# Performance work log

Hardware: AMD Instinct MI355X
Metric: run time of the kernel (lower is better)

The kernel has to match this reference:

```python
import jax, jax.numpy as jnp
import numpy as np

B, LV, HW, LT, D, H = 4, 16, 196, 32, 768, 12
DH = D // H
SCALE = 1.0 / np.sqrt(DH).astype(np.float32)


def _lin(x, W, b):
    # torch nn.Linear convention: W is [out, in]
    return x @ W.T + b


def _split_heads(x):
    # (..., D) -> (..., H, DH)
    return x.reshape(*x.shape[:-1], H, DH)


def _attn_logits(feat_q, feat_k, mask_q, mask_k, Wq, bq, Wk, bk):
    # feat_q: (B, LV, Lq, D), feat_k: (B, LV, Lk, D)
    q = _split_heads(_lin(feat_q, Wq, bq))  # b v q h d
    k = _split_heads(_lin(feat_k, Wk, bk))  # b v k h d
    logits = jnp.einsum('bvqhd,bvkhd->bvhqk', q, k)
    m = (mask_q[:, :, None] & mask_k[:, None, :])[:, None, None]  # b 1 1 q k
    return jnp.where(m, logits, -10000.0)


def setup_inputs() -> dict:
    key = jax.random.key(0)
    ks = jax.random.split(key, 12)
    inp = {
        'vid_feat': jax.random.normal(ks[0], (B, LV, HW, D), jnp.float32),
        'txt_feat': jax.random.normal(ks[1], (B, LV, LT, D), jnp.float32),
        'vid_mask': jnp.ones((B, LV), dtype=bool),
        'txt_mask': jax.random.randint(ks[2], (B, LT), 0, 2) > 0,
    }
    for i, name in enumerate(['v2v', 't2v', 't2t', 'v2t']):
        inp[name + '_W'] = jax.random.normal(ks[3 + 2 * i], (3, D, D), jnp.float32) * 0.02
        inp[name + '_b'] = jnp.zeros((3, D), jnp.float32)
    return inp


def reference(vid_feat, txt_feat, vid_mask, txt_mask,
              v2v_W, v2v_b, t2v_W, t2v_b, t2t_W, t2t_b, v2t_W, v2t_b):
    mask_hw = jnp.ones((vid_feat.shape[0], HW), dtype=bool)

    # values: concat video-keys then text-keys along the key axis
    v_value = jnp.concatenate([_lin(vid_feat, v2v_W[2], v2v_b[2]),
                               _lin(txt_feat, t2v_W[2], t2v_b[2])], axis=2)
    v_value = _split_heads(v_value)  # b v (HW+LT) h d
    t_value = jnp.concatenate([_lin(vid_feat, v2t_W[2], v2t_b[2]),
                               _lin(txt_feat, t2t_W[2], t2t_b[2])], axis=2)
    t_value = _split_heads(t_value)

    # logits (source call order: get_attn_logits(feat_k, mask_k, feat_q, mask_q, ...))
    v2v = _attn_logits(vid_feat, vid_feat, mask_hw, mask_hw, v2v_W[0], v2v_b[0], v2v_W[1], v2v_b[1])
    t2v = _attn_logits(vid_feat, txt_feat, mask_hw, txt_mask, t2v_W[0], t2v_b[0], t2v_W[1], t2v_b[1])
    v2t = _attn_logits(txt_feat, vid_feat, txt_mask, mask_hw, v2t_W[0], v2t_b[0], v2t_W[1], v2t_b[1])
    t2t = _attn_logits(txt_feat, txt_feat, txt_mask, txt_mask, t2t_W[0], t2t_b[0], t2t_W[1], t2t_b[1])

    v_logits = jnp.concatenate([v2v, t2v], axis=-1)  # b v h HW (HW+LT)
    t_logits = jnp.concatenate([v2t, t2t], axis=-1)  # b v h LT (HW+LT)

    # NOTE: source scales probabilities AFTER softmax by 1/sqrt(d_head)
    vid_out = jnp.einsum('bvhqk,bvkhd->bvqhd', jax.nn.softmax(v_logits, axis=-1) * SCALE, v_value)
    vid_out = vid_out.reshape(*vid_out.shape[:3], D)
    txt_out = jnp.einsum('bvhqk,bvkhd->bvqhd', jax.nn.softmax(t_logits, axis=-1) * SCALE, t_value)
    txt_out = txt_out.reshape(*txt_out.shape[:3], D)
    return (vid_out, txt_out)
```

## Files before the change

kernel.cpp:

```cpp
#include <hip/hip_runtime.h>

#define NBV 64
#define HWN 196
#define LTN 32
#define DIM 768
#define NH 12
#define DHD 64
#define ATT_SCALE 0.125f

typedef __attribute__((ext_vector_type(8))) __bf16 bf16x8;
typedef __attribute__((ext_vector_type(4))) float f32x4;

static __device__ __forceinline__ unsigned short f2bf(float f) {
    union { float f; unsigned u; } v; v.f = f;
    unsigned r = v.u + 0x7FFFu + ((v.u >> 16) & 1u);
    return (unsigned short)(r >> 16);
}

#define MFMA16(a, b, c) __builtin_amdgcn_mfma_f32_16x16x32_bf16((a), (b), (c), 0, 0, 0)
#define GLOAD_LDS16(g, l)                                                      \
    __builtin_amdgcn_global_load_lds(                                          \
        (const __attribute__((address_space(1))) void*)(g),                    \
        (__attribute__((address_space(3))) void*)(l), 16, 0, 0)

struct CvtCfg {
    const float* src[14];
    unsigned short* dst[14];
    int n4[14];
};

__global__ __launch_bounds__(256) void cvt_bf16(CvtCfg cfg) {
    const int e = blockIdx.y;
    const float4* s = (const float4*)cfg.src[e];
    unsigned short* d = cfg.dst[e];
    const int n4 = cfg.n4[e];
    for (int i = blockIdx.x * 256 + threadIdx.x; i < n4; i += gridDim.x * 256) {
        float4 v = s[i];
        ushort4 o;
        o.x = f2bf(v.x); o.y = f2bf(v.y); o.z = f2bf(v.z); o.w = f2bf(v.w);
        *(ushort4*)(d + (long)i * 4) = o;
    }
}

struct GemmCfg {
    const unsigned short* A[2];
    const unsigned short* W[2];
    unsigned short* out[2];
    const float* bias[2][6];
    int M[2];
};

__global__ __launch_bounds__(512, 2) void gemm_proj(GemmCfg cfg, int nb0)
{
    __shared__ __align__(16) unsigned short lds[65536];
    const int tid = threadIdx.x;
    const int lane = tid & 63, wid = tid >> 6;
    const int wm = wid >> 2, wn = wid & 3;
    const int fr = lane & 15, fg = lane >> 4;

    const int nwg = gridDim.x;
    const int orig = blockIdx.x;
    const int q = nwg >> 3, r = nwg & 7;
    const int xcd = orig & 7, lid = orig >> 3;
    const int wg = (xcd < r ? xcd * (q + 1) : r * (q + 1) + (xcd - r) * q) + lid;

    const int set = wg >= nb0;
    const int local = wg - (set ? nb0 : 0);
    const int mt = local / 18, nt = local - mt * 18;
    const int m0 = mt * 256, n0 = nt * 256;
    const int M = cfg.M[set];
    const unsigned short* __restrict__ A = cfg.A[set];
    const unsigned short* __restrict__ W = cfg.W[set];

    const int srow = tid >> 2;
    const int sxor = ((tid & 3) ^ ((tid >> 3) & 3)) * 8;
    const unsigned short* aSrc = A + (long)(m0 + srow) * DIM + sxor;
    const unsigned short* bSrc = W + (long)(n0 + srow) * DIM + sxor;
    unsigned short* ldst = lds + tid * 8;

    const int rxor = (fg ^ ((fr >> 1) & 3)) * 8;
    const int aoff = (wm * 128 + fr) * 32 + rxor;
    const int boff = 8192 + (wn * 64 + fr) * 32 + rxor;

    f32x4 acc[8][4] = {};

#define STAGE(t, s) do {                                                       \
    const unsigned short* _a = aSrc + (t) * 32;                                \
    const unsigned short* _b = bSrc + (t) * 32;                                \
    unsigned short* _d = ldst + (s) * 16384;                                   \
    GLOAD_LDS16(_a, _d);                                                       \
    GLOAD_LDS16(_a + 98304, _d + 4096);                                        \
    GLOAD_LDS16(_b, _d + 8192);                                                \
    GLOAD_LDS16(_b + 98304, _d + 12288);                                       \
} while (0)

#define COMPUTE(s) do {                                                        \
    const unsigned short* _sa = lds + (s) * 16384 + aoff;                      \
    const unsigned short* _sb = lds + (s) * 16384 + boff;                      \
    bf16x8 af[8], bg[4];                                                       \
    _Pragma("unroll") for (int m = 0; m < 4; ++m)                              \
        af[m] = *(const bf16x8*)(_sa + m * 512);                               \
    _Pragma("unroll") for (int n = 0; n < 4; ++n)                              \
        bg[n] = *(const bf16x8*)(_sb + n * 512);                               \
    _Pragma("unroll") for (int m = 4; m < 8; ++m)                              \
        af[m] = *(const bf16x8*)(_sa + m * 512);                               \
    __builtin_amdgcn_s_setprio(1);                                             \
    _Pragma("unroll") for (int m = 0; m < 4; ++m)                              \
    _Pragma("unroll") for (int n = 0; n < 4; ++n)                              \
        acc[m][n] = MFMA16(bg[n], af[m], acc[m][n]);                           \
    __builtin_amdgcn_s_setprio(0);                                             \
    __builtin_amdgcn_s_setprio(1);                                             \
    _Pragma("unroll") for (int m = 4; m < 8; ++m)                              \
    _Pragma("unroll") for (int n = 0; n < 4; ++n)                              \
        acc[m][n] = MFMA16(bg[n], af[m], acc[m][n]);                           \
    __builtin_amdgcn_s_setprio(0);                                             \
} while (0)

    STAGE(0, 0); STAGE(1, 1); STAGE(2, 2);
#pragma unroll 1
    for (int t = 0; t < 21; ++t) {
        asm volatile("s_waitcnt vmcnt(8)" ::: "memory");
        __builtin_amdgcn_s_barrier();
        STAGE(t + 3, (t + 3) & 3);
        COMPUTE(t & 3);
    }
    asm volatile("s_waitcnt vmcnt(8)" ::: "memory");
    __builtin_amdgcn_s_barrier();
    COMPUTE(1);
    asm volatile("s_waitcnt vmcnt(4)" ::: "memory");
    __builtin_amdgcn_s_barrier();
    COMPUTE(2);
    asm volatile("s_waitcnt vmcnt(0)" ::: "memory");
    __builtin_amdgcn_s_barrier();
    COMPUTE(3);

#undef STAGE
#undef COMPUTE

    const int w = nt / 3;
    const int nlb = (nt - w * 3) * 256;
    const float* bp = cfg.bias[set][w];
    unsigned short* op = cfg.out[set] + (long)w * M * DIM;
    const int colL = wn * 64;
    __builtin_amdgcn_s_barrier();
#pragma unroll
    for (int p = 0; p < 2; ++p) {
        if (wm == p) {
#pragma unroll
            for (int n = 0; n < 4; ++n) {
                float4 b4 = *(const float4*)(bp + nlb + colL + n * 16 + fg * 4);
#pragma unroll
                for (int m = 0; m < 8; ++m) {
                    ushort4 u;
                    u.x = f2bf(acc[m][n][0] + b4.x);
                    u.y = f2bf(acc[m][n][1] + b4.y);
                    u.z = f2bf(acc[m][n][2] + b4.z);
                    u.w = f2bf(acc[m][n][3] + b4.w);
                    *(ushort4*)&lds[(m * 16 + fr) * 264 + colL + n * 16 + fg * 4] = u;
                }
            }
        }
        __builtin_amdgcn_s_barrier();
#pragma unroll
        for (int i = 0; i < 8; ++i) {
            int chunk = tid + i * 512;
            int rr = chunk >> 5, cb = chunk & 31;
            bf16x8 v = *(const bf16x8*)&lds[rr * 264 + cb * 8];
            *(bf16x8*)(op + (long)(m0 + p * 128 + rr) * DIM + nlb + cb * 8) = v;
        }
        if (p == 0) __builtin_amdgcn_s_barrier();
    }
}

struct TransCfg {
    const unsigned short* src[4];
    unsigned short* dst[4];
};

__global__ __launch_bounds__(256) void transpose_v(TransCfg cfg)
{
    __shared__ unsigned short t[32][33];
    const int x = blockIdx.x;
    const int which = x >> 3;
    const int xi = x & 7;
    const int istxt = (xi == 7);
    const unsigned short* src = cfg.src[which * 2 + istxt];
    unsigned short* dst = cfg.dst[which];
    const int nrows = istxt ? LTN : HWN;
    const int colbase = istxt ? 208 : 0;
    const int rt = istxt ? 0 : xi;

    const int bv = blockIdx.z, dt = blockIdx.y;
    const int tx = threadIdx.x & 31, ty = threadIdx.x >> 5;
#pragma unroll
    for (int i = 0; i < 4; ++i) {
        int r = rt * 32 + ty + i * 8;
        t[ty + i * 8][tx] = (r < nrows)
            ? src[(long)(bv * nrows + r) * DIM + dt * 32 + tx] : (unsigned short)0;
    }
    __syncthreads();
#pragma unroll
    for (int i = 0; i < 4; ++i) {
        int d = dt * 32 + ty + i * 8;
        int rr = rt * 32 + tx;
        if (rr < nrows)
            dst[(long)(bv * DIM + d) * 256 + colbase + rr] = t[tx][ty + i * 8];
    }
}

struct AttnCfg {
    const unsigned short* QA[2];
    const unsigned short* QB[2];
    const unsigned short* KV[2];
    const unsigned short* KT[2];
    const unsigned short* Vt[2];
    float* outp[2];
};

__global__ __launch_bounds__(256, 2) void attn_kernel(AttnCfg cfg,
                                                      const int* __restrict__ tmask)
{
    __shared__ __align__(16) unsigned short P[4][16][256];
    const int tid = threadIdx.x, lane = tid & 63, wid = tid >> 6;
    const int bv = blockIdx.x, h = blockIdx.y;
    const int b = bv >> 4;
    const int sel = (blockIdx.z == 4);
    const int nq = sel ? LTN : HWN;
    const int qmask = sel;
    const unsigned short* QA = cfg.QA[sel];
    const unsigned short* QB = cfg.QB[sel];
    const unsigned short* KV = cfg.KV[sel];
    const unsigned short* KT = cfg.KT[sel];
    const unsigned short* Vt = cfg.Vt[sel];
    float* outp = cfg.outp[sel];
    const int q0 = (sel ? 0 : blockIdx.z * 64) + wid * 16;
    const int fr = lane & 15, fg = lane >> 4;

    int qr = q0 + fr; if (qr > nq - 1) qr = nq - 1;
    const unsigned short* qa_p = QA + (long)(bv * nq + qr) * DIM + h * DHD;
    const unsigned short* qb_p = QB + (long)(bv * nq + qr) * DIM + h * DHD;
    bf16x8 qa[2], qb[2];
#pragma unroll
    for (int kh = 0; kh < 2; ++kh) {
        qa[kh] = *(const bf16x8*)(qa_p + kh * 32 + fg * 8);
        qb[kh] = *(const bf16x8*)(qb_p + kh * 32 + fg * 8);
    }

    f32x4 acc[15];
#pragma unroll
    for (int kb = 0; kb < 13; ++kb) {
        int kr = kb * 16 + fr; if (kr > HWN - 1) kr = HWN - 1;
        const unsigned short* kp = KV + (long)(bv * HWN + kr) * DIM + h * DHD;
        f32x4 c = {0.f, 0.f, 0.f, 0.f};
        c = MFMA16(qa[0], *(const bf16x8*)(kp + fg * 8), c);
        c = MFMA16(qa[1], *(const bf16x8*)(kp + 32 + fg * 8), c);
        acc[kb] = c;
    }
#pragma unroll
    for (int kb = 13; kb < 15; ++kb) {
        int kr = (kb - 13) * 16 + fr;
        const unsigned short* kp = KT + (long)(bv * LTN + kr) * DIM + h * DHD;
        f32x4 c = {0.f, 0.f, 0.f, 0.f};
        c = MFMA16(qb[0], *(const bf16x8*)(kp + fg * 8), c);
        c = MFMA16(qb[1], *(const bf16x8*)(kp + 32 + fg * 8), c);
        acc[kb] = c;
    }

    bool vq[4];
#pragma unroll
    for (int j = 0; j < 4; ++j) {
        int qq = q0 + fg * 4 + j;
        if (qmask) { int qc = qq < LTN ? qq : LTN - 1; vq[j] = tmask[b * LTN + qc] != 0; }
        else vq[j] = true;
    }
#pragma unroll
    for (int kb = 0; kb < 15; ++kb) {
        int c = kb * 16 + fr;
        bool kreal = (c < HWN) || (c >= 208);
        bool kvalid = true;
        if (c >= 208) kvalid = tmask[b * LTN + (c - 208)] != 0;
#pragma unroll
        for (int j = 0; j < 4; ++j) {
            float l = acc[kb][j];
            if (!kreal) l = -3.0e38f;
            else if (!(kvalid && vq[j])) l = -10000.0f;
            acc[kb][j] = l;
        }
    }

    float mx[4], sm[4];
#pragma unroll
    for (int j = 0; j < 4; ++j) {
        float m = acc[0][j];
#pragma unroll
        for (int kb = 1; kb < 15; ++kb) m = fmaxf(m, acc[kb][j]);
        for (int s = 1; s < 16; s <<= 1) m = fmaxf(m, __shfl_xor(m, s, 64));
        mx[j] = m;
    }
#pragma unroll
    for (int j = 0; j < 4; ++j) {
        float s = 0.f;
#pragma unroll
        for (int kb = 0; kb < 15; ++kb) {
            float p = __expf(acc[kb][j] - mx[j]);
            acc[kb][j] = p;
            s += p;
        }
        for (int st = 1; st < 16; st <<= 1) s += __shfl_xor(s, st, 64);
        sm[j] = s;
    }

#pragma unroll
    for (int kb = 0; kb < 15; ++kb)
#pragma unroll
        for (int j = 0; j < 4; ++j)
            P[wid][fg * 4 + j][kb * 16 + fr] = f2bf(acc[kb][j]);
#pragma unroll
    for (int j = 0; j < 4; ++j)
        P[wid][fg * 4 + j][240 + fr] = 0;
    __syncthreads();

    f32x4 oacc[4] = {};
    const unsigned short* vt_base = Vt + (long)(bv * DIM + h * DHD) * 256;
#pragma unroll
    for (int ks = 0; ks < 8; ++ks) {
        bf16x8 a = *(const bf16x8*)&P[wid][fr][ks * 32 + fg * 8];
#pragma unroll
        for (int n = 0; n < 4; ++n) {
            const unsigned short* vp = vt_base + (long)(n * 16 + fr) * 256 + ks * 32 + fg * 8;
            oacc[n] = MFMA16(a, *(const bf16x8*)vp, oacc[n]);
        }
    }

#pragma unroll
    for (int n = 0; n < 4; ++n)
#pragma unroll
        for (int j = 0; j < 4; ++j) {
            int qq = q0 + fg * 4 + j;
            if (qq < nq)
                outp[(long)(bv * nq + qq) * DIM + h * DHD + n * 16 + fr] =
                    oacc[n][j] * (ATT_SCALE / sm[j]);
        }
}

extern "C" void kernel_launch(void* const* d_in, const int* in_sizes, int n_in,
                              void* d_out, int out_size, void* d_ws, size_t ws_size,
                              hipStream_t stream)
{
    const float* vid_feat = (const float*)d_in[0];
    const float* txt_feat = (const float*)d_in[1];
    const int*   txt_mask = (const int*)d_in[3];
    const float* v2v_W = (const float*)d_in[4];
    const float* v2v_b = (const float*)d_in[5];
    const float* t2v_W = (const float*)d_in[6];
    const float* t2v_b = (const float*)d_in[7];
    const float* t2t_W = (const float*)d_in[8];
    const float* t2t_b = (const float*)d_in[9];
    const float* v2t_W = (const float*)d_in[10];
    const float* v2t_b = (const float*)d_in[11];

    char* ws = (char*)d_ws;
    unsigned short* vid_bf   = (unsigned short*)(ws);
    unsigned short* txt_bf   = (unsigned short*)(ws + 19267584L);
    unsigned short* Wv_bf    = (unsigned short*)(ws + 22413312L);
    unsigned short* Wt_bf    = (unsigned short*)(ws + 29491200L);
    unsigned short* proj_vid = (unsigned short*)(ws + 36569088L);
    unsigned short* proj_txt = (unsigned short*)(ws + 152174592L);
    unsigned short* Vt_v     = (unsigned short*)(ws + 171048960L);
    unsigned short* Vt_t     = (unsigned short*)(ws + 196214784L);

    const long WSL = 589824;
    CvtCfg cc;
    cc.src[0] = vid_feat; cc.dst[0] = vid_bf; cc.n4[0] = 9633792 / 4;
    cc.src[1] = txt_feat; cc.dst[1] = txt_bf; cc.n4[1] = 1572864 / 4;
    const float* wsrc_v[6] = { v2v_W, v2v_W + WSL, t2v_W, v2t_W + WSL,
                               v2v_W + 2 * WSL, v2t_W + 2 * WSL };
    const float* wsrc_t[6] = { t2v_W + WSL, t2v_W + 2 * WSL, v2t_W, t2t_W,
                               t2t_W + WSL, t2t_W + 2 * WSL };
    for (int i = 0; i < 6; ++i) {
        cc.src[2 + i] = wsrc_v[i]; cc.dst[2 + i] = Wv_bf + (long)i * WSL; cc.n4[2 + i] = WSL / 4;
        cc.src[8 + i] = wsrc_t[i]; cc.dst[8 + i] = Wt_bf + (long)i * WSL; cc.n4[8 + i] = WSL / 4;
    }
    cvt_bf16<<<dim3(2048, 14), 256, 0, stream>>>(cc);

    GemmCfg gc;
    gc.A[0] = vid_bf;  gc.W[0] = Wv_bf;  gc.out[0] = proj_vid;  gc.M[0] = 12544;
    gc.A[1] = txt_bf;  gc.W[1] = Wt_bf;  gc.out[1] = proj_txt;  gc.M[1] = 2048;
    const float* bsrc_v[6] = { v2v_b, v2v_b + 768, t2v_b, v2t_b + 768,
                               v2v_b + 1536, v2t_b + 1536 };
    const float* bsrc_t[6] = { t2v_b + 768, t2v_b + 1536, v2t_b, t2t_b,
                               t2t_b + 768, t2t_b + 1536 };
    for (int i = 0; i < 6; ++i) { gc.bias[0][i] = bsrc_v[i]; gc.bias[1][i] = bsrc_t[i]; }
    gemm_proj<<<dim3(49 * 18 + 8 * 18), 512, 0, stream>>>(gc, 49 * 18);

    const long PV = 12544L * 768, PT = 2048L * 768;
    TransCfg tc;
    tc.src[0] = proj_vid + 4 * PV;  tc.src[1] = proj_txt + 1 * PT;  tc.dst[0] = Vt_v;
    tc.src[2] = proj_vid + 5 * PV;  tc.src[3] = proj_txt + 5 * PT;  tc.dst[1] = Vt_t;
    transpose_v<<<dim3(16, 24, 64), 256, 0, stream>>>(tc);

    float* out_f = (float*)d_out;
    AttnCfg ac;
    ac.QA[0] = proj_vid + 0 * PV;  ac.QB[0] = proj_vid + 2 * PV;
    ac.KV[0] = proj_vid + 1 * PV;  ac.KT[0] = proj_txt + 0 * PT;
    ac.Vt[0] = Vt_v;               ac.outp[0] = out_f;
    ac.QA[1] = proj_txt + 2 * PT;  ac.QB[1] = proj_txt + 3 * PT;
    ac.KV[1] = proj_vid + 3 * PV;  ac.KT[1] = proj_txt + 4 * PT;
    ac.Vt[1] = Vt_t;               ac.outp[1] = out_f + 9633792;
    attn_kernel<<<dim3(64, 12, 5), 256, 0, stream>>>(ac, txt_mask);
}
```

Measured before the change: 302.3 us.

## Transpose attention MFMA operands, vectorize P/output stores, shrink cvt and transpose grids

The attention kernel swaps the MFMA operand order so each lane holds one query row. That allows a single per-lane softmax with two cross-lane reductions, vectorized ushort4 P stores into a padded LDS array, and float4 output stores. Mask loads become one per-lane load plus shuffles. The __syncthreads before the P·V stage is dropped (each wave only reads its own P rows), the transpose kernel loops over all 24 column tiles per block instead of launching 24 times more blocks, and the bf16 conversion grid shrinks to 256 blocks in x. These changes cut store count, shuffle work and launch overhead, but the smaller grids may reduce parallelism.

```diff
diff --git a/kernel.cpp b/kernel.cpp
--- a/kernel.cpp
+++ b/kernel.cpp
@@ -134,14 +134,15 @@
     __builtin_amdgcn_s_barrier();
     COMPUTE(3);
 
+#undef COMPUTE
 #undef STAGE
-#undef COMPUTE
 
     const int w = nt / 3;
     const int nlb = (nt - w * 3) * 256;
     const float* bp = cfg.bias[set][w];
     unsigned short* op = cfg.out[set] + (long)w * M * DIM;
     const int colL = wn * 64;
+    asm volatile("" ::: "memory");
     __builtin_amdgcn_s_barrier();
 #pragma unroll
     for (int p = 0; p < 2; ++p) {
@@ -190,21 +191,24 @@
     const int colbase = istxt ? 208 : 0;
     const int rt = istxt ? 0 : xi;
 
-    const int bv = blockIdx.z, dt = blockIdx.y;
+    const int bv = blockIdx.z;
     const int tx = threadIdx.x & 31, ty = threadIdx.x >> 5;
-#pragma unroll
-    for (int i = 0; i < 4; ++i) {
-        int r = rt * 32 + ty + i * 8;
-        t[ty + i * 8][tx] = (r < nrows)
-            ? src[(long)(bv * nrows + r) * DIM + dt * 32 + tx] : (unsigned short)0;
-    }
-    __syncthreads();
-#pragma unroll
-    for (int i = 0; i < 4; ++i) {
-        int d = dt * 32 + ty + i * 8;
-        int rr = rt * 32 + tx;
-        if (rr < nrows)
-            dst[(long)(bv * DIM + d) * 256 + colbase + rr] = t[tx][ty + i * 8];
+    for (int dt = 0; dt < 24; ++dt) {
+#pragma unroll
+        for (int i = 0; i < 4; ++i) {
+            int r = rt * 32 + ty + i * 8;
+            t[ty + i * 8][tx] = (r < nrows)
+                ? src[(long)(bv * nrows + r) * DIM + dt * 32 + tx] : (unsigned short)0;
+        }
+        __syncthreads();
+#pragma unroll
+        for (int i = 0; i < 4; ++i) {
+            int d = dt * 32 + ty + i * 8;
+            int rr = rt * 32 + tx;
+            if (rr < nrows)
+                dst[(long)(bv * DIM + d) * 256 + colbase + rr] = t[tx][ty + i * 8];
+        }
+        __syncthreads();
     }
 }
 
@@ -220,13 +224,12 @@
 __global__ __launch_bounds__(256, 2) void attn_kernel(AttnCfg cfg,
                                                       const int* __restrict__ tmask)
 {
-    __shared__ __align__(16) unsigned short P[4][16][256];
+    __shared__ __align__(16) unsigned short P[4][16][264];
     const int tid = threadIdx.x, lane = tid & 63, wid = tid >> 6;
     const int bv = blockIdx.x, h = blockIdx.y;
     const int b = bv >> 4;
     const int sel = (blockIdx.z == 4);
     const int nq = sel ? LTN : HWN;
-    const int qmask = sel;
     const unsigned short* QA = cfg.QA[sel];
     const unsigned short* QB = cfg.QB[sel];
     const unsigned short* KV = cfg.KV[sel];
@@ -252,8 +255,8 @@
         int kr = kb * 16 + fr; if (kr > HWN - 1) kr = HWN - 1;
         const unsigned short* kp = KV + (long)(bv * HWN + kr) * DIM + h * DHD;
         f32x4 c = {0.f, 0.f, 0.f, 0.f};
-        c = MFMA16(qa[0], *(const bf16x8*)(kp + fg * 8), c);
-        c = MFMA16(qa[1], *(const bf16x8*)(kp + 32 + fg * 8), c);
+        c = MFMA16(*(const bf16x8*)(kp + fg * 8), qa[0], c);
+        c = MFMA16(*(const bf16x8*)(kp + 32 + fg * 8), qa[1], c);
         acc[kb] = c;
     }
 #pragma unroll
@@ -261,86 +264,87 @@
         int kr = (kb - 13) * 16 + fr;
         const unsigned short* kp = KT + (long)(bv * LTN + kr) * DIM + h * DHD;
         f32x4 c = {0.f, 0.f, 0.f, 0.f};
-        c = MFMA16(qb[0], *(const bf16x8*)(kp + fg * 8), c);
-        c = MFMA16(qb[1], *(const bf16x8*)(kp + 32 + fg * 8), c);
+        c = MFMA16(*(const bf16x8*)(kp + fg * 8), qb[0], c);
+        c = MFMA16(*(const bf16x8*)(kp + 32 + fg * 8), qb[1], c);
         acc[kb] = c;
     }
 
-    bool vq[4];
-#pragma unroll
-    for (int j = 0; j < 4; ++j) {
-        int qq = q0 + fg * 4 + j;
-        if (qmask) { int qc = qq < LTN ? qq : LTN - 1; vq[j] = tmask[b * LTN + qc] != 0; }
-        else vq[j] = true;
+    int tm = tmask[b * LTN + (lane & 31)];
+    bool vq = true;
+    if (sel) {
+        int qi = q0 + fr; if (qi > LTN - 1) qi = LTN - 1;
+        vq = __shfl(tm, qi, 64) != 0;
     }
 #pragma unroll
     for (int kb = 0; kb < 15; ++kb) {
-        int c = kb * 16 + fr;
-        bool kreal = (c < HWN) || (c >= 208);
-        bool kvalid = true;
-        if (c >= 208) kvalid = tmask[b * LTN + (c - 208)] != 0;
 #pragma unroll
         for (int j = 0; j < 4; ++j) {
+            int c = kb * 16 + fg * 4 + j;
+            bool kreal = (c < HWN) || (c >= 208);
+            bool kvalid = true;
+            if (c >= 208) kvalid = __shfl(tm, c - 208, 64) != 0;
             float l = acc[kb][j];
             if (!kreal) l = -3.0e38f;
-            else if (!(kvalid && vq[j])) l = -10000.0f;
+            else if (!(kvalid && vq)) l = -10000.0f;
             acc[kb][j] = l;
         }
     }
 
-    float mx[4], sm[4];
-#pragma unroll
-    for (int j = 0; j < 4; ++j) {
-        float m = acc[0][j];
-#pragma unroll
-        for (int kb = 1; kb < 15; ++kb) m = fmaxf(m, acc[kb][j]);
-        for (int s = 1; s < 16; s <<= 1) m = fmaxf(m, __shfl_xor(m, s, 64));
-        mx[j] = m;
-    }
-#pragma unroll
-    for (int j = 0; j < 4; ++j) {
-        float s = 0.f;
-#pragma unroll
-        for (int kb = 0; kb < 15; ++kb) {
-            float p = __expf(acc[kb][j] - mx[j]);
+    float mx = -3.0e38f;
+#pragma unroll
+    for (int kb = 0; kb < 15; ++kb)
+#pragma unroll
+        for (int j = 0; j < 4; ++j) mx = fmaxf(mx, acc[kb][j]);
+    mx = fmaxf(mx, __shfl_xor(mx, 16, 64));
+    mx = fmaxf(mx, __shfl_xor(mx, 32, 64));
+    float s = 0.f;
+#pragma unroll
+    for (int kb = 0; kb < 15; ++kb)
+#pragma unroll
+        for (int j = 0; j < 4; ++j) {
+            float p = __expf(acc[kb][j] - mx);
             acc[kb][j] = p;
             s += p;
         }
-        for (int st = 1; st < 16; st <<= 1) s += __shfl_xor(s, st, 64);
-        sm[j] = s;
-    }
-
-#pragma unroll
-    for (int kb = 0; kb < 15; ++kb)
-#pragma unroll
-        for (int j = 0; j < 4; ++j)
-            P[wid][fg * 4 + j][kb * 16 + fr] = f2bf(acc[kb][j]);
-#pragma unroll
-    for (int j = 0; j < 4; ++j)
-        P[wid][fg * 4 + j][240 + fr] = 0;
-    __syncthreads();
+    s += __shfl_xor(s, 16, 64);
+    s += __shfl_xor(s, 32, 64);
+
+    unsigned short* pw = &P[wid][fr][0];
+#pragma unroll
+    for (int kb = 0; kb < 15; ++kb) {
+        ushort4 u;
+        u.x = f2bf(acc[kb][0]); u.y = f2bf(acc[kb][1]);
+        u.z = f2bf(acc[kb][2]); u.w = f2bf(acc[kb][3]);
+        *(ushort4*)(pw + kb * 16 + fg * 4) = u;
+    }
+    {
+        ushort4 z = {0, 0, 0, 0};
+        *(ushort4*)(pw + 240 + fg * 4) = z;
+    }
 
     f32x4 oacc[4] = {};
-    const unsigned short* vt_base = Vt + (long)(bv * DIM + h * DHD) * 256;
+    const unsigned short* vt_base = Vt + ((long)bv * DIM + h * DHD) * 256;
 #pragma unroll
     for (int ks = 0; ks < 8; ++ks) {
-        bf16x8 a = *(const bf16x8*)&P[wid][fr][ks * 32 + fg * 8];
+        bf16x8 pf = *(const bf16x8*)(pw + ks * 32 + fg * 8);
 #pragma unroll
         for (int n = 0; n < 4; ++n) {
             const unsigned short* vp = vt_base + (long)(n * 16 + fr) * 256 + ks * 32 + fg * 8;
-            oacc[n] = MFMA16(a, *(const bf16x8*)vp, oacc[n]);
-        }
-    }
-
-#pragma unroll
-    for (int n = 0; n < 4; ++n)
-#pragma unroll
-        for (int j = 0; j < 4; ++j) {
-            int qq = q0 + fg * 4 + j;
-            if (qq < nq)
-                outp[(long)(bv * nq + qq) * DIM + h * DHD + n * 16 + fr] =
-                    oacc[n][j] * (ATT_SCALE / sm[j]);
-        }
+            oacc[n] = MFMA16(*(const bf16x8*)vp, pf, oacc[n]);
+        }
+    }
+
+    if (q0 + fr < nq) {
+        float inv = ATT_SCALE / s;
+        float* ob = outp + (long)(bv * nq + q0 + fr) * DIM + h * DHD;
+#pragma unroll
+        for (int n = 0; n < 4; ++n) {
+            float4 o;
+            o.x = oacc[n][0] * inv; o.y = oacc[n][1] * inv;
+            o.z = oacc[n][2] * inv; o.w = oacc[n][3] * inv;
+            *(float4*)(ob + n * 16 + fg * 4) = o;
+        }
+    }
 }
 
 extern "C" void kernel_launch(void* const* d_in, const int* in_sizes, int n_in,
@@ -381,7 +385,7 @@
         cc.src[2 + i] = wsrc_v[i]; cc.dst[2 + i] = Wv_bf + (long)i * WSL; cc.n4[2 + i] = WSL / 4;
         cc.src[8 + i] = wsrc_t[i]; cc.dst[8 + i] = Wt_bf + (long)i * WSL; cc.n4[8 + i] = WSL / 4;
     }
-    cvt_bf16<<<dim3(2048, 14), 256, 0, stream>>>(cc);
+    cvt_bf16<<<dim3(256, 14), 256, 0, stream>>>(cc);
 
     GemmCfg gc;
     gc.A[0] = vid_bf;  gc.W[0] = Wv_bf;  gc.out[0] = proj_vid;  gc.M[0] = 12544;
@@ -397,7 +401,7 @@
     TransCfg tc;
     tc.src[0] = proj_vid + 4 * PV;  tc.src[1] = proj_txt + 1 * PT;  tc.dst[0] = Vt_v;
     tc.src[2] = proj_vid + 5 * PV;  tc.src[3] = proj_txt + 5 * PT;  tc.dst[1] = Vt_t;
-    transpose_v<<<dim3(16, 24, 64), 256, 0, stream>>>(tc);
+    transpose_v<<<dim3(16, 1, 64), 256, 0, stream>>>(tc);
 
     float* out_f = (float*)d_out;
     AttnCfg ac;
```

Result: slower. 312.9 us (+3.5%).
